# Kernel optimization log

Hardware: AMD Instinct MI355X
Metric: run time of the kernel (lower is better)

The kernel has to match this reference:

```python
import jax, jax.numpy as jnp
import numpy as np

N_NODES = 150000
N_EDGES = 2400000
F_IN = 128
HID = 32
N_CLS = 1


def setup_inputs() -> dict:
    key = jax.random.key(0)
    ks = jax.random.split(key, 8)
    x = jax.random.normal(ks[0], (N_NODES, F_IN), dtype=jnp.float32)
    edge_index = jax.random.randint(ks[1], (2, N_EDGES), 0, N_NODES, dtype=jnp.int64)
    # Glorot-ish scaled weights
    W1 = jax.random.normal(ks[2], (F_IN, HID), dtype=jnp.float32) * (1.0 / np.sqrt(F_IN))
    b1 = jnp.zeros((HID,), dtype=jnp.float32)
    W2 = jax.random.normal(ks[3], (HID, HID), dtype=jnp.float32) * (1.0 / np.sqrt(HID))
    b2 = jnp.zeros((HID,), dtype=jnp.float32)
    W3 = jax.random.normal(ks[4], (HID, N_CLS), dtype=jnp.float32) * (1.0 / np.sqrt(HID))
    b3 = jnp.zeros((N_CLS,), dtype=jnp.float32)
    return {"x": x, "edge_index": edge_index, "W1": W1, "b1": b1,
            "W2": W2, "b2": b2, "W3": W3, "b3": b3}


def reference(x, edge_index, W1, b1, W2, b2, W3, b3):
    # GCNConv (Kipf & Welling): add self-loops, symmetric normalization,
    # transform-then-aggregate. Dropout omitted (inference: training=False).
    n = x.shape[0]
    loop = jnp.arange(n, dtype=edge_index.dtype)
    src = jnp.concatenate([edge_index[0], loop])  # [E+N]
    dst = jnp.concatenate([edge_index[1], loop])  # [E+N]
    deg = jax.ops.segment_sum(jnp.ones(src.shape[0], x.dtype), dst, num_segments=n)
    deg_inv_sqrt = jax.lax.rsqrt(jnp.maximum(deg, 1.0))  # deg >= 1 (self-loops)
    norm = (deg_inv_sqrt[src] * deg_inv_sqrt[dst])[:, None]  # [E+N, 1]

    def gcn_conv(h, W, b):
        h = h @ W                                   # [N, out]
        msg = h[src] * norm                         # gather + scale  [E+N, out]
        return jax.ops.segment_sum(msg, dst, num_segments=n) + b

    h = jax.nn.relu(gcn_conv(x, W1, b1))
    h = jax.nn.relu(gcn_conv(h, W2, b2))
    return jax.nn.sigmoid(gcn_conv(h, W3, b3))      # [N, 1]
```

## Files before the change

kernel.cpp:

```cpp
#include <hip/hip_runtime.h>
#include <hip/hip_fp16.h>
#include <math.h>

#define F_IN 128
#define HID  32

#define NPB   256
#define MAXNB 1024
#define EPB   8192
#define BLK_E 1024
#define BLK_C 512

#define XPAD  132

__device__ __forceinline__ void fma4(float4& a, float s, const float4& w) {
    a.x = fmaf(s, w.x, a.x);
    a.y = fmaf(s, w.y, a.y);
    a.z = fmaf(s, w.z, a.z);
    a.w = fmaf(s, w.w, a.w);
}

__device__ __forceinline__ void add4(float4& a, const float4& v) {
    a.x += v.x; a.y += v.y; a.z += v.z; a.w += v.w;
}

__device__ __forceinline__ float4 shx4(float4 v, int m) {
    float4 r;
    r.x = __shfl_xor(v.x, m);
    r.y = __shfl_xor(v.y, m);
    r.z = __shfl_xor(v.z, m);
    r.w = __shfl_xor(v.w, m);
    return r;
}

__device__ __forceinline__ float4 ldh4(const __half* p) {
    uint2 u = *(const uint2*)p;
    __half2 h0 = *(__half2*)&u.x;
    __half2 h1 = *(__half2*)&u.y;
    float2 f0 = __half22float2(h0);
    float2 f1 = __half22float2(h1);
    return make_float4(f0.x, f0.y, f1.x, f1.y);
}
__device__ __forceinline__ void sth4(__half* p, float4 v) {
    __half2 h0 = __floats2half2_rn(v.x, v.y);
    __half2 h1 = __floats2half2_rn(v.z, v.w);
    uint2 u;
    u.x = *(unsigned*)&h0;
    u.y = *(unsigned*)&h1;
    *(uint2*)p = u;
}


__global__ __launch_bounds__(BLK_E) void k_bhist(const int* __restrict__ dst,
                                                 int* __restrict__ bin_hist,
                                                 int* __restrict__ hb,
                                                 int e, int nbuckets) {
    __shared__ int h[MAXNB];
    int tid = threadIdx.x;
    for (int i = tid; i < nbuckets; i += BLK_E) h[i] = 0;
    __syncthreads();
    int base = blockIdx.x * EPB;
    if (base + EPB <= e) {
        const int4* d4 = (const int4*)(dst + base);
#pragma unroll
        for (int i = tid; i < EPB / 4; i += BLK_E) {
            int4 v = d4[i];
            atomicAdd(&h[v.x >> 8], 1);
            atomicAdd(&h[v.y >> 8], 1);
            atomicAdd(&h[v.z >> 8], 1);
            atomicAdd(&h[v.w >> 8], 1);
        }
    } else {
        int end = e;
        for (int i = base + tid; i < end; i += BLK_E)
            atomicAdd(&h[dst[i] >> 8], 1);
    }
    __syncthreads();
    size_t hbase = (size_t)blockIdx.x * nbuckets;
    for (int i = tid; i < nbuckets; i += BLK_E) {
        int c = h[i];
        if (c) atomicAdd(&bin_hist[i], c);
        hb[hbase + i] = c;
    }
}

__global__ __launch_bounds__(1024) void k_bscan(const int* __restrict__ bin_hist,
                                                int* __restrict__ bin_off,
                                                int* __restrict__ bin_cur,
                                                int* __restrict__ offsets,
                                                int nbuckets, int n, int e) {
    __shared__ int sh[MAXNB];
    int t = threadIdx.x;
    int v = (t < nbuckets) ? bin_hist[t] : 0;
    sh[t] = v; __syncthreads();
    for (int off = 1; off < MAXNB; off <<= 1) {
        int a = (t >= off) ? sh[t - off] : 0;
        __syncthreads();
        sh[t] += a;
        __syncthreads();
    }
    int excl = sh[t] - v;
    if (t < nbuckets) { bin_off[t] = excl; bin_cur[t] = excl; }
    if (t == 0) { bin_off[nbuckets] = e; offsets[n] = e; }
}

__global__ __launch_bounds__(BLK_E) void k_bpart(const int* __restrict__ src,
                                                 const int* __restrict__ dst,
                                                 int* __restrict__ bin_cur,
                                                 unsigned* __restrict__ tmp,
                                                 const int* __restrict__ hb,
                                                 int e, int nbuckets) {
    __shared__ int h[MAXNB];
    __shared__ int lc[MAXNB];
    int tid = threadIdx.x;
    size_t hbase = (size_t)blockIdx.x * nbuckets;
    for (int i = tid; i < nbuckets; i += BLK_E) {
        int c = hb[hbase + i];
        h[i] = c ? atomicAdd(&bin_cur[i], c) : 0;
        lc[i] = 0;
    }
    __syncthreads();
    int base = blockIdx.x * EPB;
    bool full = (base + EPB <= e);
    if (full) {
        const int4* s4 = (const int4*)(src + base);
        const int4* d4 = (const int4*)(dst + base);
#pragma unroll
        for (int i = tid; i < EPB / 4; i += BLK_E) {
            int4 sv = s4[i];
            int4 dv = d4[i];
            int b0 = dv.x >> 8; int r0 = atomicAdd(&lc[b0], 1);
            tmp[h[b0] + r0] = (unsigned)sv.x | ((unsigned)(dv.x & (NPB - 1)) << 18);
            int b1 = dv.y >> 8; int r1 = atomicAdd(&lc[b1], 1);
            tmp[h[b1] + r1] = (unsigned)sv.y | ((unsigned)(dv.y & (NPB - 1)) << 18);
            int b2 = dv.z >> 8; int r2 = atomicAdd(&lc[b2], 1);
            tmp[h[b2] + r2] = (unsigned)sv.z | ((unsigned)(dv.z & (NPB - 1)) << 18);
            int b3 = dv.w >> 8; int r3 = atomicAdd(&lc[b3], 1);
            tmp[h[b3] + r3] = (unsigned)sv.w | ((unsigned)(dv.w & (NPB - 1)) << 18);
        }
    } else {
        for (int i = base + tid; i < e; i += BLK_E) {
            int d = dst[i];
            int b = d >> 8;
            int r = atomicAdd(&lc[b], 1);
            tmp[h[b] + r] = (unsigned)src[i] | ((unsigned)(d & (NPB - 1)) << 18);
        }
    }
}

__global__ __launch_bounds__(BLK_C) void k_bcsr(const unsigned* __restrict__ tmp,
                                                const int* __restrict__ bin_off,
                                                int* __restrict__ es,
                                                int* __restrict__ offsets,
                                                float* __restrict__ dis, int n) {
    __shared__ int cnt[NPB];
    __shared__ int sh[NPB];
    __shared__ int cur[NPB];
    int b = blockIdx.x, t = threadIdx.x;
    if (t < NPB) cnt[t] = 0;
    __syncthreads();
    int s0 = bin_off[b], s1 = bin_off[b + 1];
    for (int i = s0 + t; i < s1; i += BLK_C)
        atomicAdd(&cnt[(tmp[i] >> 18) & (NPB - 1)], 1);
    __syncthreads();
    int v = (t < NPB) ? cnt[t] : 0;
    if (t < NPB) sh[t] = v;
    __syncthreads();
    for (int off = 1; off < NPB; off <<= 1) {
        int a = (t < NPB && t >= off) ? sh[t - off] : 0;
        __syncthreads();
        if (t < NPB) sh[t] += a;
        __syncthreads();
    }
    if (t < NPB) {
        int excl = sh[t] - v;
        int node = b * NPB + t;
        if (node < n) {
            offsets[node] = s0 + excl;
            dis[node] = rsqrtf((float)(v + 1));
        }
        cur[t] = excl;
    }
    __syncthreads();
    for (int i = s0 + t; i < s1; i += BLK_C) {
        unsigned w = tmp[i];
        int dl = (w >> 18) & (NPB - 1);
        int r = atomicAdd(&cur[dl], 1);
        es[s0 + r] = (int)(w & 0x3FFFFu);
    }
}


__global__ __launch_bounds__(256) void k_gemm1(const float* __restrict__ x,
                                               const float* __restrict__ W,
                                               const float* __restrict__ dis,
                                               __half* __restrict__ u, int n) {
    __shared__ float Ws[F_IN * HID];
    __shared__ float Xs[64 * XPAD];
    int tid = threadIdx.x;
    for (int i = tid; i < F_IN * HID; i += 256) Ws[i] = W[i];
    int node0 = blockIdx.x * 64;
#pragma unroll
    for (int it = 0; it < 8; ++it) {
        int c  = it * 256 + tid;
        int r  = c >> 5;
        int c4 = c & 31;
        int gr = node0 + r;
        if (gr >= n) gr = n - 1;
        float4 v = *(const float4*)&x[(size_t)gr * F_IN + c4 * 4];
        *(float4*)&Xs[r * XPAD + c4 * 4] = v;
    }
    int cg = tid & 7, gq = tid >> 3;
    float4 acc[2];
    acc[0] = make_float4(0.f, 0.f, 0.f, 0.f);
    acc[1] = make_float4(0.f, 0.f, 0.f, 0.f);
    __syncthreads();
#pragma unroll 4
    for (int ks = 0; ks < 32; ++ks) {
        float4 xv[2];
        xv[0] = *(const float4*)&Xs[gq * XPAD + ks * 4];
        xv[1] = *(const float4*)&Xs[(gq + 32) * XPAD + ks * 4];
        float4 w0 = *(const float4*)&Ws[(ks * 4 + 0) * HID + cg * 4];
        float4 w1 = *(const float4*)&Ws[(ks * 4 + 1) * HID + cg * 4];
        float4 w2 = *(const float4*)&Ws[(ks * 4 + 2) * HID + cg * 4];
        float4 w3 = *(const float4*)&Ws[(ks * 4 + 3) * HID + cg * 4];
#pragma unroll
        for (int m = 0; m < 2; ++m) {
            fma4(acc[m], xv[m].x, w0);
            fma4(acc[m], xv[m].y, w1);
            fma4(acc[m], xv[m].z, w2);
            fma4(acc[m], xv[m].w, w3);
        }
    }
#pragma unroll
    for (int m = 0; m < 2; ++m) {
        int node = node0 + gq + 32 * m;
        if (node < n) {
            float ds = dis[node];
            float4 r;
            r.x = acc[m].x * ds; r.y = acc[m].y * ds;
            r.z = acc[m].z * ds; r.w = acc[m].w * ds;
            sth4(&u[(size_t)node * HID + cg * 4], r);
        }
    }
}


__global__ __launch_bounds__(256) void k_gather32_g2(const __half* __restrict__ uh,
                                                     const int* __restrict__ es,
                                                     const int* __restrict__ offsets,
                                                     const float* __restrict__ dis,
                                                     const float* __restrict__ b,
                                                     const float* __restrict__ W2,
                                                     __half* __restrict__ u2, int n) {
    __shared__ float Ws[HID * HID];
    int tid = threadIdx.x;
    for (int i = tid; i < HID * HID; i += 256) Ws[i] = W2[i];
    __syncthreads();
    int t = blockIdx.x * 256 + tid;
    int node = t >> 3, q = t & 7;
    if (node >= n) return;
    int s0 = offsets[node];
    int s1 = offsets[node + 1];
    float4 acc = ldh4(&uh[(size_t)node * HID + q * 4]);
    int ei = s0;
    for (; ei + 8 <= s1; ei += 8) {
        int e0 = es[ei], e1 = es[ei + 1], e2 = es[ei + 2], e3 = es[ei + 3];
        int e4 = es[ei + 4], e5 = es[ei + 5], e6 = es[ei + 6], e7 = es[ei + 7];
        float4 v0 = ldh4(&uh[(size_t)e0 * HID + q * 4]);
        float4 v1 = ldh4(&uh[(size_t)e1 * HID + q * 4]);
        float4 v2 = ldh4(&uh[(size_t)e2 * HID + q * 4]);
        float4 v3 = ldh4(&uh[(size_t)e3 * HID + q * 4]);
        float4 v4 = ldh4(&uh[(size_t)e4 * HID + q * 4]);
        float4 v5 = ldh4(&uh[(size_t)e5 * HID + q * 4]);
        float4 v6 = ldh4(&uh[(size_t)e6 * HID + q * 4]);
        float4 v7 = ldh4(&uh[(size_t)e7 * HID + q * 4]);
        acc.x += ((v0.x + v1.x) + (v2.x + v3.x)) + ((v4.x + v5.x) + (v6.x + v7.x));
        acc.y += ((v0.y + v1.y) + (v2.y + v3.y)) + ((v4.y + v5.y) + (v6.y + v7.y));
        acc.z += ((v0.z + v1.z) + (v2.z + v3.z)) + ((v4.z + v5.z) + (v6.z + v7.z));
        acc.w += ((v0.w + v1.w) + (v2.w + v3.w)) + ((v4.w + v5.w) + (v6.w + v7.w));
    }
    for (; ei + 4 <= s1; ei += 4) {
        int e0 = es[ei], e1 = es[ei + 1], e2 = es[ei + 2], e3 = es[ei + 3];
        float4 v0 = ldh4(&uh[(size_t)e0 * HID + q * 4]);
        float4 v1 = ldh4(&uh[(size_t)e1 * HID + q * 4]);
        float4 v2 = ldh4(&uh[(size_t)e2 * HID + q * 4]);
        float4 v3 = ldh4(&uh[(size_t)e3 * HID + q * 4]);
        acc.x += (v0.x + v1.x) + (v2.x + v3.x);
        acc.y += (v0.y + v1.y) + (v2.y + v3.y);
        acc.z += (v0.z + v1.z) + (v2.z + v3.z);
        acc.w += (v0.w + v1.w) + (v2.w + v3.w);
    }
    for (; ei < s1; ++ei) {
        int s = es[ei];
        float4 v = ldh4(&uh[(size_t)s * HID + q * 4]);
        add4(acc, v);
    }
    float ds = dis[node];
    float4 r;
    r.x = fmaxf(fmaf(ds, acc.x, b[q * 4 + 0]), 0.0f);
    r.y = fmaxf(fmaf(ds, acc.y, b[q * 4 + 1]), 0.0f);
    r.z = fmaxf(fmaf(ds, acc.z, b[q * 4 + 2]), 0.0f);
    r.w = fmaxf(fmaf(ds, acc.w, b[q * 4 + 3]), 0.0f);

    float4 o1 = shx4(r, 1);
    float4 L0 = (q & 1) ? o1 : r;
    float4 L1 = (q & 1) ? r  : o1;
    float4 M0 = shx4(L0, 2);
    float4 M1 = shx4(L1, 2);
    float4 P0 = (q & 2) ? M0 : L0;
    float4 P1 = (q & 2) ? M1 : L1;
    float4 P2 = (q & 2) ? L0 : M0;
    float4 P3 = (q & 2) ? L1 : M1;
    float4 Q0 = shx4(P0, 4);
    float4 Q1 = shx4(P1, 4);
    float4 Q2 = shx4(P2, 4);
    float4 Q3 = shx4(P3, 4);
    float4 H0 = (q & 4) ? Q0 : P0;
    float4 H1 = (q & 4) ? Q1 : P1;
    float4 H2 = (q & 4) ? Q2 : P2;
    float4 H3 = (q & 4) ? Q3 : P3;
    float4 H4 = (q & 4) ? P0 : Q0;
    float4 H5 = (q & 4) ? P1 : Q1;
    float4 H6 = (q & 4) ? P2 : Q2;
    float4 H7 = (q & 4) ? P3 : Q3;

    float4 oacc = make_float4(0.f, 0.f, 0.f, 0.f);
#define G2_STEP(Hj, j) { \
    float4 w0 = *(const float4*)&Ws[((j) * 4 + 0) * HID + q * 4]; \
    float4 w1 = *(const float4*)&Ws[((j) * 4 + 1) * HID + q * 4]; \
    float4 w2 = *(const float4*)&Ws[((j) * 4 + 2) * HID + q * 4]; \
    float4 w3 = *(const float4*)&Ws[((j) * 4 + 3) * HID + q * 4]; \
    fma4(oacc, Hj.x, w0); fma4(oacc, Hj.y, w1); \
    fma4(oacc, Hj.z, w2); fma4(oacc, Hj.w, w3); }
    G2_STEP(H0, 0) G2_STEP(H1, 1) G2_STEP(H2, 2) G2_STEP(H3, 3)
    G2_STEP(H4, 4) G2_STEP(H5, 5) G2_STEP(H6, 6) G2_STEP(H7, 7)
#undef G2_STEP
    float4 w;
    w.x = oacc.x * ds; w.y = oacc.y * ds;
    w.z = oacc.z * ds; w.w = oacc.w * ds;
    sth4(&u2[(size_t)node * HID + q * 4], w);
}

__global__ __launch_bounds__(256) void k_gather32_dot(const __half* __restrict__ uh,
                                                      const int* __restrict__ es,
                                                      const int* __restrict__ offsets,
                                                      const float* __restrict__ dis,
                                                      const float* __restrict__ b,
                                                      const float* __restrict__ W3,
                                                      float* __restrict__ s, int n) {
    int t = blockIdx.x * 256 + threadIdx.x;
    int node = t >> 3, q = t & 7;
    if (node >= n) return;
    int s0 = offsets[node];
    int s1 = offsets[node + 1];
    float4 acc = ldh4(&uh[(size_t)node * HID + q * 4]);
    int ei = s0;
    for (; ei + 8 <= s1; ei += 8) {
        int e0 = es[ei], e1 = es[ei + 1], e2 = es[ei + 2], e3 = es[ei + 3];
        int e4 = es[ei + 4], e5 = es[ei + 5], e6 = es[ei + 6], e7 = es[ei + 7];
        float4 v0 = ldh4(&uh[(size_t)e0 * HID + q * 4]);
        float4 v1 = ldh4(&uh[(size_t)e1 * HID + q * 4]);
        float4 v2 = ldh4(&uh[(size_t)e2 * HID + q * 4]);
        float4 v3 = ldh4(&uh[(size_t)e3 * HID + q * 4]);
        float4 v4 = ldh4(&uh[(size_t)e4 * HID + q * 4]);
        float4 v5 = ldh4(&uh[(size_t)e5 * HID + q * 4]);
        float4 v6 = ldh4(&uh[(size_t)e6 * HID + q * 4]);
        float4 v7 = ldh4(&uh[(size_t)e7 * HID + q * 4]);
        acc.x += ((v0.x + v1.x) + (v2.x + v3.x)) + ((v4.x + v5.x) + (v6.x + v7.x));
        acc.y += ((v0.y + v1.y) + (v2.y + v3.y)) + ((v4.y + v5.y) + (v6.y + v7.y));
        acc.z += ((v0.z + v1.z) + (v2.z + v3.z)) + ((v4.z + v5.z) + (v6.z + v7.z));
        acc.w += ((v0.w + v1.w) + (v2.w + v3.w)) + ((v4.w + v5.w) + (v6.w + v7.w));
    }
    for (; ei + 4 <= s1; ei += 4) {
        int e0 = es[ei], e1 = es[ei + 1], e2 = es[ei + 2], e3 = es[ei + 3];
        float4 v0 = ldh4(&uh[(size_t)e0 * HID + q * 4]);
        float4 v1 = ldh4(&uh[(size_t)e1 * HID + q * 4]);
        float4 v2 = ldh4(&uh[(size_t)e2 * HID + q * 4]);
        float4 v3 = ldh4(&uh[(size_t)e3 * HID + q * 4]);
        acc.x += (v0.x + v1.x) + (v2.x + v3.x);
        acc.y += (v0.y + v1.y) + (v2.y + v3.y);
        acc.z += (v0.z + v1.z) + (v2.z + v3.z);
        acc.w += (v0.w + v1.w) + (v2.w + v3.w);
    }
    for (; ei < s1; ++ei) {
        int sc = es[ei];
        float4 v = ldh4(&uh[(size_t)sc * HID + q * 4]);
        add4(acc, v);
    }
    float ds = dis[node];
    float4 r;
    r.x = fmaxf(fmaf(ds, acc.x, b[q * 4 + 0]), 0.0f);
    r.y = fmaxf(fmaf(ds, acc.y, b[q * 4 + 1]), 0.0f);
    r.z = fmaxf(fmaf(ds, acc.z, b[q * 4 + 2]), 0.0f);
    r.w = fmaxf(fmaf(ds, acc.w, b[q * 4 + 3]), 0.0f);
    float p = r.x * W3[q * 4 + 0] + r.y * W3[q * 4 + 1]
            + r.z * W3[q * 4 + 2] + r.w * W3[q * 4 + 3];
    p += __shfl_down(p, 4, 8);
    p += __shfl_down(p, 2, 8);
    p += __shfl_down(p, 1, 8);
    if (q == 0) s[node] = p * ds;
}

__global__ void k_gather1(const float* __restrict__ sv, const int* __restrict__ es,
                          const int* __restrict__ offsets, const float* __restrict__ dis,
                          const float* __restrict__ b3, float* __restrict__ out, int n) {
    int d = blockIdx.x * 256 + threadIdx.x;
    if (d >= n) return;
    float acc = sv[d];
    int s0 = offsets[d], s1 = offsets[d + 1];
    int ei = s0;
    for (; ei + 4 <= s1; ei += 4) {
        float v0 = sv[es[ei]], v1 = sv[es[ei + 1]];
        float v2 = sv[es[ei + 2]], v3 = sv[es[ei + 3]];
        acc += (v0 + v1) + (v2 + v3);
    }
    for (; ei < s1; ++ei) acc += sv[es[ei]];
    float z = dis[d] * acc + b3[0];
    out[d] = 1.0f / (1.0f + expf(-z));
}


extern "C" void kernel_launch(void* const* d_in, const int* in_sizes, int n_in,
                              void* d_out, int out_size, void* d_ws, size_t ws_size,
                              hipStream_t stream) {
    const float* x  = (const float*)d_in[0];
    const int*   ei = (const int*)d_in[1];
    const float* W1 = (const float*)d_in[2];
    const float* b1 = (const float*)d_in[3];
    const float* W2 = (const float*)d_in[4];
    const float* b2 = (const float*)d_in[5];
    const float* W3 = (const float*)d_in[6];
    const float* b3 = (const float*)d_in[7];
    float* out = (float*)d_out;

    int n = out_size;
    int e = in_sizes[1] / 2;
    const int* src = ei;
    const int* dst = ei + e;

    int nbuckets = (n + NPB - 1) / NPB;
    int gEb      = (e + EPB - 1) / EPB;

    __half* A       = (__half*)d_ws;
    __half* B       = A + (size_t)n * HID;
    float* dis      = (float*)(B + (size_t)n * HID);
    float* Cs       = dis + n;
    int*   offsets  = (int*)(Cs + n);
    int*   es       = offsets + (n + 1);
    int*   bin_hist = es + e;
    int*   bin_off  = bin_hist + nbuckets;
    int*   bin_cur  = bin_off + (nbuckets + 1);
    int*   hb       = bin_cur + nbuckets;
    unsigned* tmp   = (unsigned*)B;

    dim3 blk(256);
    int gN    = (n + 255) / 256;
    int gN8   = (n * 8 + 255) / 256;
    int g64   = (n + 63) / 64;

    hipMemsetAsync(bin_hist, 0, (size_t)nbuckets * sizeof(int), stream);
    k_bhist<<<gEb, dim3(BLK_E), 0, stream>>>(dst, bin_hist, hb, e, nbuckets);
    k_bscan<<<1, 1024, 0, stream>>>(bin_hist, bin_off, bin_cur, offsets, nbuckets, n, e);
    k_bpart<<<gEb, dim3(BLK_E), 0, stream>>>(src, dst, bin_cur, tmp, hb, e, nbuckets);
    k_bcsr <<<nbuckets, dim3(BLK_C), 0, stream>>>(tmp, bin_off, es, offsets, dis, n);

    k_gemm1      <<<g64, blk, 0, stream>>>(x, W1, dis, A, n);
    k_gather32_g2<<<gN8, blk, 0, stream>>>(A, es, offsets, dis, b1, W2, B, n);

    k_gather32_dot<<<gN8, blk, 0, stream>>>(B, es, offsets, dis, b2, W3, Cs, n);

    k_gather1<<<gN, blk, 0, stream>>>(Cs, es, offsets, dis, b3, out, n);
}
```

Baseline: 300.8 us.

## Fold bucket scan into partition and CSR kernels; resize buckets to 256

Drops the standalone single-block bucket-scan kernel. Each k_bpart and k_bcsr block now recomputes the prefix sum over bucket counts itself, which removes one launch and its serialization point. Bucket size changes from 256 to 586 nodes so there are at most 256 buckets, edges per block rise to 9376, and k_bcsr moves to 1024 threads with vectorized uint4 reads of tmp. The cost is a redundant 1024-wide scan in every block, integer division instead of shifts, and larger per-bucket CSR work.

Result: faster. 291.1 us (-3.2%).

```diff
diff --git a/kernel.cpp b/kernel.cpp
--- a/kernel.cpp
+++ b/kernel.cpp
@@ -5,11 +5,10 @@
 #define F_IN 128
 #define HID  32
 
-#define NPB   256
-#define MAXNB 1024
-#define EPB   8192
+#define NPB   586
+#define NBK   256
+#define EPB   9376
 #define BLK_E 1024
-#define BLK_C 512
 
 #define XPAD  132
 
@@ -55,121 +54,132 @@
                                                  int* __restrict__ bin_hist,
                                                  int* __restrict__ hb,
                                                  int e, int nbuckets) {
-    __shared__ int h[MAXNB];
+    __shared__ int h[NBK];
     int tid = threadIdx.x;
-    for (int i = tid; i < nbuckets; i += BLK_E) h[i] = 0;
+    if (tid < nbuckets) h[tid] = 0;
     __syncthreads();
     int base = blockIdx.x * EPB;
     if (base + EPB <= e) {
         const int4* d4 = (const int4*)(dst + base);
-#pragma unroll
         for (int i = tid; i < EPB / 4; i += BLK_E) {
             int4 v = d4[i];
-            atomicAdd(&h[v.x >> 8], 1);
-            atomicAdd(&h[v.y >> 8], 1);
-            atomicAdd(&h[v.z >> 8], 1);
-            atomicAdd(&h[v.w >> 8], 1);
+            atomicAdd(&h[v.x / NPB], 1);
+            atomicAdd(&h[v.y / NPB], 1);
+            atomicAdd(&h[v.z / NPB], 1);
+            atomicAdd(&h[v.w / NPB], 1);
         }
     } else {
-        int end = e;
-        for (int i = base + tid; i < end; i += BLK_E)
-            atomicAdd(&h[dst[i] >> 8], 1);
-    }
-    __syncthreads();
-    size_t hbase = (size_t)blockIdx.x * nbuckets;
-    for (int i = tid; i < nbuckets; i += BLK_E) {
-        int c = h[i];
-        if (c) atomicAdd(&bin_hist[i], c);
-        hb[hbase + i] = c;
-    }
-}
-
-__global__ __launch_bounds__(1024) void k_bscan(const int* __restrict__ bin_hist,
-                                                int* __restrict__ bin_off,
-                                                int* __restrict__ bin_cur,
-                                                int* __restrict__ offsets,
-                                                int nbuckets, int n, int e) {
-    __shared__ int sh[MAXNB];
-    int t = threadIdx.x;
-    int v = (t < nbuckets) ? bin_hist[t] : 0;
-    sh[t] = v; __syncthreads();
-    for (int off = 1; off < MAXNB; off <<= 1) {
-        int a = (t >= off) ? sh[t - off] : 0;
-        __syncthreads();
-        sh[t] += a;
-        __syncthreads();
-    }
-    int excl = sh[t] - v;
-    if (t < nbuckets) { bin_off[t] = excl; bin_cur[t] = excl; }
-    if (t == 0) { bin_off[nbuckets] = e; offsets[n] = e; }
-}
+        for (int i = base + tid; i < e; i += BLK_E)
+            atomicAdd(&h[dst[i] / NPB], 1);
+    }
+    __syncthreads();
+    int hbase = blockIdx.x * nbuckets;
+    if (tid < nbuckets) {
+        int c = h[tid];
+        if (c) atomicAdd(&bin_hist[tid], c);
+        hb[hbase + tid] = c;
+    }
+}
+
+#define BP_ONE(S, D) { \
+    int b_ = (D) / NPB; int dl_ = (D) - b_ * NPB; \
+    int r_ = atomicAdd(&lc[b_], 1); \
+    tmp[h[b_] + r_] = (unsigned)(S) | ((unsigned)dl_ << 18); }
 
 __global__ __launch_bounds__(BLK_E) void k_bpart(const int* __restrict__ src,
                                                  const int* __restrict__ dst,
+                                                 const int* __restrict__ bin_hist,
                                                  int* __restrict__ bin_cur,
                                                  unsigned* __restrict__ tmp,
                                                  const int* __restrict__ hb,
                                                  int e, int nbuckets) {
-    __shared__ int h[MAXNB];
-    __shared__ int lc[MAXNB];
-    int tid = threadIdx.x;
-    size_t hbase = (size_t)blockIdx.x * nbuckets;
-    for (int i = tid; i < nbuckets; i += BLK_E) {
-        int c = hb[hbase + i];
-        h[i] = c ? atomicAdd(&bin_cur[i], c) : 0;
-        lc[i] = 0;
+    __shared__ int sh[BLK_E];
+    __shared__ int h[NBK];
+    __shared__ int lc[NBK];
+    int t = threadIdx.x;
+    int hv = (t < nbuckets) ? bin_hist[t] : 0;
+    sh[t] = hv; __syncthreads();
+    for (int off = 1; off < BLK_E; off <<= 1) {
+        int a = (t >= off) ? sh[t - off] : 0;
+        __syncthreads();
+        sh[t] += a;
+        __syncthreads();
+    }
+    int hbase = blockIdx.x * nbuckets;
+    if (t < nbuckets) {
+        int boff = sh[t] - hv;
+        int c = hb[hbase + t];
+        h[t] = c ? boff + atomicAdd(&bin_cur[t], c) : 0;
+        lc[t] = 0;
     }
     __syncthreads();
     int base = blockIdx.x * EPB;
-    bool full = (base + EPB <= e);
-    if (full) {
+    if (base + EPB <= e) {
         const int4* s4 = (const int4*)(src + base);
         const int4* d4 = (const int4*)(dst + base);
-#pragma unroll
-        for (int i = tid; i < EPB / 4; i += BLK_E) {
+        for (int i = t; i < EPB / 4; i += BLK_E) {
             int4 sv = s4[i];
             int4 dv = d4[i];
-            int b0 = dv.x >> 8; int r0 = atomicAdd(&lc[b0], 1);
-            tmp[h[b0] + r0] = (unsigned)sv.x | ((unsigned)(dv.x & (NPB - 1)) << 18);
-            int b1 = dv.y >> 8; int r1 = atomicAdd(&lc[b1], 1);
-            tmp[h[b1] + r1] = (unsigned)sv.y | ((unsigned)(dv.y & (NPB - 1)) << 18);
-            int b2 = dv.z >> 8; int r2 = atomicAdd(&lc[b2], 1);
-            tmp[h[b2] + r2] = (unsigned)sv.z | ((unsigned)(dv.z & (NPB - 1)) << 18);
-            int b3 = dv.w >> 8; int r3 = atomicAdd(&lc[b3], 1);
-            tmp[h[b3] + r3] = (unsigned)sv.w | ((unsigned)(dv.w & (NPB - 1)) << 18);
+            BP_ONE(sv.x, dv.x)
+            BP_ONE(sv.y, dv.y)
+            BP_ONE(sv.z, dv.z)
+            BP_ONE(sv.w, dv.w)
         }
     } else {
-        for (int i = base + tid; i < e; i += BLK_E) {
+        for (int i = base + t; i < e; i += BLK_E) {
             int d = dst[i];
-            int b = d >> 8;
-            int r = atomicAdd(&lc[b], 1);
-            tmp[h[b] + r] = (unsigned)src[i] | ((unsigned)(d & (NPB - 1)) << 18);
-        }
-    }
-}
-
-__global__ __launch_bounds__(BLK_C) void k_bcsr(const unsigned* __restrict__ tmp,
-                                                const int* __restrict__ bin_off,
+            BP_ONE(src[i], d)
+        }
+    }
+}
+#undef BP_ONE
+
+__global__ __launch_bounds__(BLK_E) void k_bcsr(const unsigned* __restrict__ tmp,
+                                                const int* __restrict__ bin_hist,
                                                 int* __restrict__ es,
                                                 int* __restrict__ offsets,
-                                                float* __restrict__ dis, int n) {
+                                                float* __restrict__ dis,
+                                                int n, int nbuckets, int e) {
+    __shared__ int sh[BLK_E];
     __shared__ int cnt[NPB];
-    __shared__ int sh[NPB];
     __shared__ int cur[NPB];
+    __shared__ int sb[2];
     int b = blockIdx.x, t = threadIdx.x;
+    int hv = (t < nbuckets) ? bin_hist[t] : 0;
     if (t < NPB) cnt[t] = 0;
-    __syncthreads();
-    int s0 = bin_off[b], s1 = bin_off[b + 1];
-    for (int i = s0 + t; i < s1; i += BLK_C)
-        atomicAdd(&cnt[(tmp[i] >> 18) & (NPB - 1)], 1);
+    sh[t] = hv; __syncthreads();
+    for (int off = 1; off < BLK_E; off <<= 1) {
+        int a = (t >= off) ? sh[t - off] : 0;
+        __syncthreads();
+        sh[t] += a;
+        __syncthreads();
+    }
+    if (t == b) { sb[0] = sh[t] - hv; sb[1] = sh[t]; }
+    if (b == nbuckets - 1 && t == 0) offsets[n] = e;
+    __syncthreads();
+    int s0 = sb[0], s1 = sb[1];
+    int a0 = (s0 + 3) & ~3; if (a0 > s1) a0 = s1;
+    int a1 = s1 & ~3;       if (a1 < a0) a1 = a0;
+    for (int i = s0 + t; i < a0; i += BLK_E)
+        atomicAdd(&cnt[(tmp[i] >> 18) & 1023], 1);
+    int nv = (a1 - a0) >> 2;
+    const uint4* t4 = (const uint4*)(tmp + a0);
+    for (int i = t; i < nv; i += BLK_E) {
+        uint4 w = t4[i];
+        atomicAdd(&cnt[(w.x >> 18) & 1023], 1);
+        atomicAdd(&cnt[(w.y >> 18) & 1023], 1);
+        atomicAdd(&cnt[(w.z >> 18) & 1023], 1);
+        atomicAdd(&cnt[(w.w >> 18) & 1023], 1);
+    }
+    for (int i = a1 + t; i < s1; i += BLK_E)
+        atomicAdd(&cnt[(tmp[i] >> 18) & 1023], 1);
     __syncthreads();
     int v = (t < NPB) ? cnt[t] : 0;
-    if (t < NPB) sh[t] = v;
-    __syncthreads();
-    for (int off = 1; off < NPB; off <<= 1) {
-        int a = (t < NPB && t >= off) ? sh[t - off] : 0;
-        __syncthreads();
-        if (t < NPB) sh[t] += a;
+    sh[t] = v; __syncthreads();
+    for (int off = 1; off < BLK_E; off <<= 1) {
+        int a = (t >= off) ? sh[t - off] : 0;
+        __syncthreads();
+        sh[t] += a;
         __syncthreads();
     }
     if (t < NPB) {
@@ -182,9 +192,26 @@
         cur[t] = excl;
     }
     __syncthreads();
-    for (int i = s0 + t; i < s1; i += BLK_C) {
+    for (int i = s0 + t; i < a0; i += BLK_E) {
         unsigned w = tmp[i];
-        int dl = (w >> 18) & (NPB - 1);
+        int dl = (w >> 18) & 1023;
+        int r = atomicAdd(&cur[dl], 1);
+        es[s0 + r] = (int)(w & 0x3FFFFu);
+    }
+    for (int i = t; i < nv; i += BLK_E) {
+        uint4 w = t4[i];
+        int d0 = (w.x >> 18) & 1023; int r0 = atomicAdd(&cur[d0], 1);
+        es[s0 + r0] = (int)(w.x & 0x3FFFFu);
+        int d1 = (w.y >> 18) & 1023; int r1 = atomicAdd(&cur[d1], 1);
+        es[s0 + r1] = (int)(w.y & 0x3FFFFu);
+        int d2 = (w.z >> 18) & 1023; int r2 = atomicAdd(&cur[d2], 1);
+        es[s0 + r2] = (int)(w.z & 0x3FFFFu);
+        int d3 = (w.w >> 18) & 1023; int r3 = atomicAdd(&cur[d3], 1);
+        es[s0 + r3] = (int)(w.w & 0x3FFFFu);
+    }
+    for (int i = a1 + t; i < s1; i += BLK_E) {
+        unsigned w = tmp[i];
+        int dl = (w >> 18) & 1023;
         int r = atomicAdd(&cur[dl], 1);
         es[s0 + r] = (int)(w & 0x3FFFFu);
     }
@@ -449,8 +476,7 @@
     int*   offsets  = (int*)(Cs + n);
     int*   es       = offsets + (n + 1);
     int*   bin_hist = es + e;
-    int*   bin_off  = bin_hist + nbuckets;
-    int*   bin_cur  = bin_off + (nbuckets + 1);
+    int*   bin_cur  = bin_hist + nbuckets;
     int*   hb       = bin_cur + nbuckets;
     unsigned* tmp   = (unsigned*)B;
 
@@ -459,11 +485,10 @@
     int gN8   = (n * 8 + 255) / 256;
     int g64   = (n + 63) / 64;
 
-    hipMemsetAsync(bin_hist, 0, (size_t)nbuckets * sizeof(int), stream);
+    hipMemsetAsync(bin_hist, 0, (size_t)(2 * nbuckets) * sizeof(int), stream);
     k_bhist<<<gEb, dim3(BLK_E), 0, stream>>>(dst, bin_hist, hb, e, nbuckets);
-    k_bscan<<<1, 1024, 0, stream>>>(bin_hist, bin_off, bin_cur, offsets, nbuckets, n, e);
-    k_bpart<<<gEb, dim3(BLK_E), 0, stream>>>(src, dst, bin_cur, tmp, hb, e, nbuckets);
-    k_bcsr <<<nbuckets, dim3(BLK_C), 0, stream>>>(tmp, bin_off, es, offsets, dis, n);
+    k_bpart<<<gEb, dim3(BLK_E), 0, stream>>>(src, dst, bin_hist, bin_cur, tmp, hb, e, nbuckets);
+    k_bcsr <<<nbuckets, dim3(BLK_E), 0, stream>>>(tmp, bin_hist, es, offsets, dis, n, nbuckets, e);
 
     k_gemm1      <<<g64, blk, 0, stream>>>(x, W1, dis, A, n);
     k_gather32_g2<<<gN8, blk, 0, stream>>>(A, es, offsets, dis, b1, W2, B, n);
```
